# Performance work log

Hardware: AMD Instinct MI355X
Metric: run time of the kernel (lower is better)

## Reference

```python
import jax, jax.numpy as jnp
import numpy as np

B, V, F = 128, 256, 64      # batch, vertices, features-per-vertex
NS, NLR, K, NOUT = 4, 64, 40, 128
F_EFF = 2 * F               # cat_means doubles feature dim


def setup_inputs() -> dict:
    key = jax.random.key(0)
    k0, k1, k2 = jax.random.split(key, 3)
    x = jax.random.normal(k0, (B, V, F), dtype=jnp.float32)
    # f_slr: single Linear(F_EFF, NS+NLR) + ReLU (f_slr_depth=1)
    W_slr = jax.random.normal(k1, (F_EFF, NS + NLR), dtype=jnp.float32) / np.sqrt(F_EFF).astype(np.float32)
    b_slr = jnp.zeros((NS + NLR,), dtype=jnp.float32)
    # f_out: single Linear(F_EFF + 2*NLR, NOUT) + ReLU (f_out_depth=1, 2 agg methods)
    fin = F_EFF + 2 * NLR
    W_out = jax.random.normal(k2, (fin, NOUT), dtype=jnp.float32) / np.sqrt(fin).astype(np.float32)
    b_out = jnp.zeros((NOUT,), dtype=jnp.float32)
    return {"x": x, "W_slr": W_slr, "b_slr": b_slr, "W_out": W_out, "b_out": b_out}


def reference(x, W_slr, b_slr, W_out, b_out):
    # cat_means: append per-event feature means (broadcast over vertices)
    x = jnp.concatenate([x, jnp.broadcast_to(x.mean(axis=1, keepdims=True), x.shape)], axis=-1)  # (B,V,2F)
    slr = jax.nn.relu(x @ W_slr + b_slr)                    # (B,V,NS+NLR)
    s, lr = slr[..., :NS], slr[..., NS:]
    # pairwise squared distances in latent space (potential only needs d^2, so
    # we skip the sqrt: exp(-10*d^2) == exp(-10*d2), and kNN order is identical)
    diff = s[:, :, None, :] - s[:, None, :, :]              # (B,V,V,NS)
    d2 = jnp.sum(diff * diff, axis=-1)                      # (B,V,V)
    _, idx = jax.lax.top_k(-d2, K)                          # (B,V,K) k smallest (incl. self)
    d2k = jnp.take_along_axis(d2, idx, axis=2)              # (B,V,K)
    lr_nb = jax.vmap(lambda l, i: l[i])(lr, idx)            # (B,V,K,NLR)
    v = jnp.exp(-10.0 * d2k)                                # potential exp(-10 d^2)
    ft = lr_nb * v[..., None]                               # (B,V,K,NLR)
    fp = jnp.concatenate([x, ft.mean(axis=2), ft.max(axis=2)], axis=-1)  # (B,V,2F+2NLR)
    return jax.nn.relu(fp @ W_out + b_out)                  # (B,V,NOUT)
```

## Files before the change

kernel.cpp:

```cpp
#include <hip/hip_runtime.h>

constexpr int Bn = 128, Vn = 256, Fn = 64;
constexpr int NSLR = 68, NSn = 4, NLRn = 64;
constexpr int Kn = 40, NOUTn = 128;
constexpr int ROWS = Bn * Vn;
constexpr int KB2 = 192;

typedef __attribute__((ext_vector_type(8))) short short8;
typedef __attribute__((ext_vector_type(4))) float f32x4;

__device__ __forceinline__ int mbcnt64(unsigned long long m) {
  return __builtin_amdgcn_mbcnt_hi((unsigned)(m >> 32),
         __builtin_amdgcn_mbcnt_lo((unsigned)(m & 0xFFFFFFFFull), 0));
}
__device__ __forceinline__ unsigned short rneb(float v) {
  unsigned u = __float_as_uint(v);
  unsigned r = u + 0x7FFFu + ((u >> 16) & 1u);
  return (unsigned short)(r >> 16);
}
__device__ __forceinline__ float bf2f(unsigned short h) {
  return __uint_as_float(((unsigned)h) << 16);
}
#define GL_LDS(gp, lp) __builtin_amdgcn_global_load_lds( \
    (const __attribute__((address_space(1))) void*)(gp), \
    (__attribute__((address_space(3))) void*)(lp), 16, 0, 0)

__global__ __launch_bounds__(256) void kprep(
    const float* __restrict__ x,
    const float* __restrict__ W_slr, const float* __restrict__ b_slr,
    const float* __restrict__ W_out, const float* __restrict__ b_out,
    short* __restrict__ xhi, short* __restrict__ xlo,
    short* __restrict__ wt1h, short* __restrict__ wt1l, short* __restrict__ wt2,
    float* __restrict__ bias1, float* __restrict__ bias2) {
  const int blk = blockIdx.x, t = threadIdx.x;
  if (blk >= Bn) {
    const int col = blk - Bn;
    if (t < 64) {
      float val = (col < NSLR) ? W_slr[t * NSLR + col] : 0.f;
      unsigned short h = rneb(val);
      wt1h[col * 64 + t] = (short)h;
      wt1l[col * 64 + t] = (short)rneb(val - bf2f(h));
    } else {
      int k = t - 64;
      int row = (k < 64) ? k : 64 + k;
      wt2[col * KB2 + k] = (short)rneb(W_out[row * NOUTn + col]);
    }
    return;
  }
  const int b = blk;
  const int f4 = t & 15, vg = t >> 4;
  const float4* xb = (const float4*)(x + (size_t)b * 16384);
  float4 sum = make_float4(0.f, 0.f, 0.f, 0.f);
  for (int i = 0; i < 16; ++i) {
    int v = vg * 16 + i;
    float4 val = xb[v * 16 + f4];
    sum.x += val.x; sum.y += val.y; sum.z += val.z; sum.w += val.w;
    unsigned short h0 = rneb(val.x), h1 = rneb(val.y), h2 = rneb(val.z), h3 = rneb(val.w);
    short4 hi = {(short)h0, (short)h1, (short)h2, (short)h3};
    short4 lo = {(short)rneb(val.x - bf2f(h0)), (short)rneb(val.y - bf2f(h1)),
                 (short)rneb(val.z - bf2f(h2)), (short)rneb(val.w - bf2f(h3))};
    size_t o = (size_t)b * 4096 + v * 16 + f4;
    ((short4*)xhi)[o] = hi;
    ((short4*)xlo)[o] = lo;
  }
  __shared__ float4 ps[16][16];
  __shared__ float xms[64];
  ps[vg][f4] = sum;
  __syncthreads();
  if (t < 16) {
    float4 m = ps[0][t];
    for (int g = 1; g < 16; ++g) {
      float4 v = ps[g][t];
      m.x += v.x; m.y += v.y; m.z += v.z; m.w += v.w;
    }
    m.x *= (1.f / 256.f); m.y *= (1.f / 256.f); m.z *= (1.f / 256.f); m.w *= (1.f / 256.f);
    ((float4*)xms)[t] = m;
  }
  __syncthreads();
  if (t < 128) {
    float acc = b_out[t];
    for (int f = 0; f < 64; ++f) acc = fmaf(xms[f], W_out[(64 + f) * NOUTn + t], acc);
    bias2[b * 128 + t] = acc;
  } else {
    int c = t - 128;
    if (c < NSLR) {
      float acc = b_slr[c];
      for (int f = 0; f < 64; ++f) acc = fmaf(xms[f], W_slr[(64 + f) * NSLR + c], acc);
      bias1[b * 128 + c] = acc;
    }
  }
}

__global__ __launch_bounds__(256) void kgemm1(
    const short* __restrict__ xhi, const short* __restrict__ xlo,
    const short* __restrict__ wt1h, const short* __restrict__ wt1l,
    const float* __restrict__ bias1,
    float* __restrict__ s_ws, float* __restrict__ lr_ws) {
  __shared__ __align__(16) short Ah[4096], Al[4096], Bh[8192], Bl[1024];
  const int t = threadIdx.x, l = t & 63, w = t >> 6;
  const int wr = w >> 1, wc = w & 1;
  const int rowBase = blockIdx.x * 64;
  const int b = rowBase >> 8;
  const int lr8 = l >> 3, ul = (l & 7) ^ lr8;

#pragma unroll
  for (int rep = 0; rep < 2; ++rep) {
    const int seg = w + rep * 4;
    size_t o = (size_t)(rowBase + seg * 8 + lr8) * 64 + ul * 8;
    GL_LDS(xhi + o, &Ah[seg * 512]);
    GL_LDS(xlo + o, &Al[seg * 512]);
  }
#pragma unroll
  for (int rep = 0; rep < 4; ++rep) {
    const int seg = w + rep * 4;
    size_t o = (size_t)(seg * 8 + lr8) * 64 + ul * 8;
    GL_LDS(wt1h + o, &Bh[seg * 512]);
  }
  if (w < 2) {
    size_t o = (size_t)(w * 8 + lr8) * 64 + ul * 8;
    GL_LDS(wt1l + o, &Bl[w * 512]);
  }
  __syncthreads();

  f32x4 acc[2][4];
#pragma unroll
  for (int mf = 0; mf < 2; ++mf)
#pragma unroll
    for (int nf = 0; nf < 4; ++nf) acc[mf][nf] = (f32x4)(0.f);

#pragma unroll
  for (int ks = 0; ks < 2; ++ks) {
    short8 ah[2], bh[4];
#pragma unroll
    for (int mf = 0; mf < 2; ++mf) {
      int row = wr * 32 + mf * 16 + (l & 15);
      int pu = (ks * 4 + (l >> 4)) ^ (row & 7);
      ah[mf] = *(const short8*)&Ah[row * 64 + pu * 8];
    }
#pragma unroll
    for (int nf = 0; nf < 4; ++nf) {
      int col = wc * 64 + nf * 16 + (l & 15);
      int pu = (ks * 4 + (l >> 4)) ^ (col & 7);
      bh[nf] = *(const short8*)&Bh[col * 64 + pu * 8];
    }
#pragma unroll
    for (int mf = 0; mf < 2; ++mf)
#pragma unroll
      for (int nf = 0; nf < 4; ++nf)
        acc[mf][nf] = __builtin_amdgcn_mfma_f32_16x16x32_bf16(ah[mf], bh[nf], acc[mf][nf], 0, 0, 0);
    if (wc == 0) {
      int col0 = l & 15;
      int puc = (ks * 4 + (l >> 4)) ^ (col0 & 7);
      short8 bl0 = *(const short8*)&Bl[col0 * 64 + puc * 8];
#pragma unroll
      for (int mf = 0; mf < 2; ++mf) {
        int row = wr * 32 + mf * 16 + (l & 15);
        int pu = (ks * 4 + (l >> 4)) ^ (row & 7);
        short8 al = *(const short8*)&Al[row * 64 + pu * 8];
        acc[mf][0] = __builtin_amdgcn_mfma_f32_16x16x32_bf16(ah[mf], bl0, acc[mf][0], 0, 0, 0);
        acc[mf][0] = __builtin_amdgcn_mfma_f32_16x16x32_bf16(al, bh[0], acc[mf][0], 0, 0, 0);
      }
    }
  }
#pragma unroll
  for (int mf = 0; mf < 2; ++mf)
#pragma unroll
    for (int nf = 0; nf < 4; ++nf) {
      const int col = wc * 64 + nf * 16 + (l & 15);
      if (col < NSLR) {
        const float bia = bias1[b * 128 + col];
#pragma unroll
        for (int r = 0; r < 4; ++r) {
          int row = rowBase + wr * 32 + mf * 16 + (l >> 4) * 4 + r;
          float vv = acc[mf][nf][r] + bia;
          vv = vv > 0.f ? vv : 0.f;
          if (col < NSn) s_ws[b * 1024 + col * 256 + (row & 255)] = vv;
          else           lr_ws[(size_t)row * NLRn + (col - NSn)] = vv;
        }
      }
    }
}

__global__ __launch_bounds__(256) void kgemm2(
    const short* __restrict__ xhi, const short* __restrict__ fm,
    const short* __restrict__ fx, const short* __restrict__ wt2,
    const float* __restrict__ bias2, float* __restrict__ outp) {
  __shared__ __align__(16) short As[4096], Bs[8192];
  const int t = threadIdx.x, l = t & 63, w = t >> 6;
  const int wr = w >> 1, wc = w & 1;
  const int rowBase = blockIdx.x * 64;
  const int b = rowBase >> 8;
  const int lr8 = l >> 3, ul = (l & 7) ^ lr8;

  f32x4 acc[2][4];
#pragma unroll
  for (int mf = 0; mf < 2; ++mf)
#pragma unroll
    for (int nf = 0; nf < 4; ++nf) acc[mf][nf] = (f32x4)(0.f);

#pragma unroll
  for (int kc = 0; kc < 3; ++kc) {
    __syncthreads();
    const short* asrc = (kc == 0) ? xhi : (kc == 1) ? fm : fx;
#pragma unroll
    for (int rep = 0; rep < 2; ++rep) {
      const int seg = w + rep * 4;
      size_t o = (size_t)(rowBase + seg * 8 + lr8) * 64 + ul * 8;
      GL_LDS(asrc + o, &As[seg * 512]);
    }
#pragma unroll
    for (int rep = 0; rep < 4; ++rep) {
      const int seg = w + rep * 4;
      size_t o = (size_t)(seg * 8 + lr8) * KB2 + kc * 64 + ul * 8;
      GL_LDS(wt2 + o, &Bs[seg * 512]);
    }
    __syncthreads();
#pragma unroll
    for (int ks = 0; ks < 2; ++ks) {
      short8 a[2], bb[4];
#pragma unroll
      for (int mf = 0; mf < 2; ++mf) {
        int row = wr * 32 + mf * 16 + (l & 15);
        int pu = (ks * 4 + (l >> 4)) ^ (row & 7);
        a[mf] = *(const short8*)&As[row * 64 + pu * 8];
      }
#pragma unroll
      for (int nf = 0; nf < 4; ++nf) {
        int col = wc * 64 + nf * 16 + (l & 15);
        int pu = (ks * 4 + (l >> 4)) ^ (col & 7);
        bb[nf] = *(const short8*)&Bs[col * 64 + pu * 8];
      }
#pragma unroll
      for (int mf = 0; mf < 2; ++mf)
#pragma unroll
        for (int nf = 0; nf < 4; ++nf)
          acc[mf][nf] = __builtin_amdgcn_mfma_f32_16x16x32_bf16(a[mf], bb[nf], acc[mf][nf], 0, 0, 0);
    }
  }
#pragma unroll
  for (int mf = 0; mf < 2; ++mf)
#pragma unroll
    for (int nf = 0; nf < 4; ++nf) {
      const int col = wc * 64 + nf * 16 + (l & 15);
      const float bia = bias2[b * 128 + col];
#pragma unroll
      for (int r = 0; r < 4; ++r) {
        int row = rowBase + wr * 32 + mf * 16 + (l >> 4) * 4 + r;
        float vv = acc[mf][nf][r] + bia;
        outp[(size_t)row * NOUTn + col] = vv > 0.f ? vv : 0.f;
      }
    }
}

__device__ __forceinline__ int cntlt(const unsigned* kbr, unsigned c) {
  return __popcll(__ballot(kbr[0] < c)) + __popcll(__ballot(kbr[1] < c)) +
         __popcll(__ballot(kbr[2] < c)) + __popcll(__ballot(kbr[3] < c));
}

__global__ __launch_bounds__(256) void kselect(const float* __restrict__ s_ws,
                                               const float* __restrict__ lr_ws,
                                               short* __restrict__ fm,
                                               short* __restrict__ fx) {
  __shared__ float sT[4][256];
  __shared__ unsigned int lst[4][4][Kn];
  const int id = blockIdx.x;
  const int xcd = id & 7;
  const int rrx = id >> 3;
  const int b = xcd + 8 * (rrx & 15);
  const int seg = rrx >> 4;
  const int t = threadIdx.x, lane = t & 63, w = t >> 6;

  {
    const float* sb = s_ws + b * 1024;
    sT[0][t] = sb[t]; sT[1][t] = sb[256 + t];
    sT[2][t] = sb[512 + t]; sT[3][t] = sb[768 + t];
  }
  __syncthreads();

  float sj[4][4];
#pragma unroll
  for (int q = 0; q < 4; ++q)
#pragma unroll
    for (int c = 0; c < 4; ++c) sj[q][c] = sT[c][q * 64 + lane];

  const float C = -14.4269504088896340736f;
  unsigned kb[4][4];
  float vv[4][4];
#pragma unroll
  for (int r = 0; r < 4; ++r) {
    const int i = seg * 16 + w * 4 + r;
    const float si0 = sT[0][i], si1 = sT[1][i], si2 = sT[2][i], si3 = sT[3][i];
#pragma unroll
    for (int q = 0; q < 4; ++q) {
      float d0 = sj[q][0] - si0;
      float d1 = sj[q][1] - si1;
      float d2_ = sj[q][2] - si2;
      float d3 = sj[q][3] - si3;
      float dd = ((d0 * d0 + d1 * d1) + d2_ * d2_) + d3 * d3;
      kb[r][q] = __float_as_uint(dd);
      vv[r][q] = exp2f(C * dd);
    }
  }
  unsigned T[4] = {0u, 0u, 0u, 0u};
#pragma unroll 1
  for (int bit = 30; bit >= 0; --bit) {
    const unsigned m = 1u << bit;
    unsigned c0 = T[0] | m, c1 = T[1] | m, c2 = T[2] | m, c3 = T[3] | m;
    int n0 = cntlt(kb[0], c0);
    int n1 = cntlt(kb[1], c1);
    int n2 = cntlt(kb[2], c2);
    int n3 = cntlt(kb[3], c3);
    T[0] = (n0 < Kn) ? c0 : T[0];
    T[1] = (n1 < Kn) ? c1 : T[1];
    T[2] = (n2 < Kn) ? c2 : T[2];
    T[3] = (n3 < Kn) ? c3 : T[3];
  }
#pragma unroll
  for (int r = 0; r < 4; ++r) {
    const unsigned Tr = T[r];
    int nlt = cntlt(kb[r], Tr);
    int rem = Kn - nlt;
    int base = 0, ecum = 0;
#pragma unroll
    for (int q = 0; q < 4; ++q) {
      bool lt = kb[r][q] < Tr;
      bool eq = kb[r][q] == Tr;
      unsigned long long meq = __ballot(eq);
      int eqrank = ecum + mbcnt64(meq);
      bool sel = lt || (eq && (eqrank < rem));
      unsigned long long msel = __ballot(sel);
      int pos = base + mbcnt64(msel);
      if (sel)
        lst[w][r][pos] = (__float_as_uint(vv[r][q]) & 0xFFFFFF00u) | (unsigned)(q * 64 + lane);
      base += __popcll(msel);
      ecum += __popcll(meq);
    }
  }
  float accm[4] = {0.f, 0.f, 0.f, 0.f};
  float accx[4] = {0.f, 0.f, 0.f, 0.f};
  const float* lrb = lr_ws + (size_t)b * (256 * NLRn) + lane;
#pragma unroll 4
  for (int tt = 0; tt < Kn; ++tt) {
#pragma unroll
    for (int r = 0; r < 4; ++r) {
      unsigned p = lst[w][r][tt];
      int j = p & 0xFF;
      float v = __uint_as_float(p & 0xFFFFFF00u);
      float tv = v * lrb[j * NLRn];
      accm[r] += tv;
      accx[r] = fmaxf(accx[r], tv);
    }
  }
#pragma unroll
  for (int r = 0; r < 4; ++r) {
    const int i = seg * 16 + w * 4 + r;
    size_t ro = ((size_t)(b * 256 + i)) * 64 + lane;
    fm[ro] = (short)rneb(accm[r] * (1.f / 40.f));
    fx[ro] = (short)rneb(accx[r]);
  }
}

extern "C" void kernel_launch(void* const* d_in, const int* in_sizes, int n_in,
                              void* d_out, int out_size, void* d_ws, size_t ws_size,
                              hipStream_t stream) {
  const float* x = (const float*)d_in[0];
  const float* W_slr = (const float*)d_in[1];
  const float* b_slr = (const float*)d_in[2];
  const float* W_out = (const float*)d_in[3];
  const float* b_out = (const float*)d_in[4];
  float* out = (float*)d_out;

  char* p = (char*)d_ws;
  auto take = [&](size_t bytes) { char* c = p; p += (bytes + 255) & ~(size_t)255; return c; };
  short* xhi = (short*)take((size_t)ROWS * 64 * 2);
  short* xlo = (short*)take((size_t)ROWS * 64 * 2);
  short* wt1h = (short*)take(128 * 64 * 2);
  short* wt1l = (short*)take(128 * 64 * 2);
  short* wt2 = (short*)take(128 * KB2 * 2);
  float* bias1 = (float*)take(Bn * 128 * 4);
  float* bias2 = (float*)take(Bn * 128 * 4);
  float* s_ws = (float*)take(Bn * 1024 * 4);
  float* lr_ws = (float*)take((size_t)ROWS * 64 * 4);
  short* fm = (short*)take((size_t)ROWS * 64 * 2);
  short* fx = (short*)take((size_t)ROWS * 64 * 2);

  kprep<<<256, 256, 0, stream>>>(x, W_slr, b_slr, W_out, b_out,
                                 xhi, xlo, wt1h, wt1l, wt2, bias1, bias2);
  kgemm1<<<ROWS / 64, 256, 0, stream>>>(xhi, xlo, wt1h, wt1l, bias1, s_ws, lr_ws);
  kselect<<<Bn * 16, 256, 0, stream>>>(s_ws, lr_ws, fm, fx);
  kgemm2<<<ROWS / 64, 256, 0, stream>>>(xhi, fm, fx, wt2, bias2, out);
}
```

Baseline: 130.6 us.

## Store lr features as bf16, stage them in LDS for kNN gather, prefetch all gemm2 K-chunks

kgemm1 now writes the lr latent features as bf16 instead of fp32, which halves that intermediate's size. kselect copies the whole per-batch bf16 lr block (32 KB) into LDS with async global-to-LDS loads and gathers neighbours from LDS. Each lane processes two packed features for half-wave rows and writes packed bf16 pairs. kgemm2 loads all three K chunks into separate LDS buffers up front with a single barrier instead of two barriers per chunk. This trades extra LDS use, which may lower occupancy, and some lr precision for less global traffic and synchronisation.

```diff
diff --git a/kernel.cpp b/kernel.cpp
--- a/kernel.cpp
+++ b/kernel.cpp
@@ -95,7 +95,7 @@
     const short* __restrict__ xhi, const short* __restrict__ xlo,
     const short* __restrict__ wt1h, const short* __restrict__ wt1l,
     const float* __restrict__ bias1,
-    float* __restrict__ s_ws, float* __restrict__ lr_ws) {
+    float* __restrict__ s_ws, unsigned short* __restrict__ lr_bf) {
   __shared__ __align__(16) short Ah[4096], Al[4096], Bh[8192], Bl[1024];
   const int t = threadIdx.x, l = t & 63, w = t >> 6;
   const int wr = w >> 1, wc = w & 1;
@@ -175,7 +175,7 @@
           float vv = acc[mf][nf][r] + bia;
           vv = vv > 0.f ? vv : 0.f;
           if (col < NSn) s_ws[b * 1024 + col * 256 + (row & 255)] = vv;
-          else           lr_ws[(size_t)row * NLRn + (col - NSn)] = vv;
+          else           lr_bf[(size_t)row * NLRn + (col - NSn)] = rneb(vv);
         }
       }
     }
@@ -185,36 +185,39 @@
     const short* __restrict__ xhi, const short* __restrict__ fm,
     const short* __restrict__ fx, const short* __restrict__ wt2,
     const float* __restrict__ bias2, float* __restrict__ outp) {
-  __shared__ __align__(16) short As[4096], Bs[8192];
+  __shared__ __align__(16) short As[3][4096], Bs[3][8192];
   const int t = threadIdx.x, l = t & 63, w = t >> 6;
   const int wr = w >> 1, wc = w & 1;
   const int rowBase = blockIdx.x * 64;
   const int b = rowBase >> 8;
   const int lr8 = l >> 3, ul = (l & 7) ^ lr8;
 
-  f32x4 acc[2][4];
-#pragma unroll
-  for (int mf = 0; mf < 2; ++mf)
-#pragma unroll
-    for (int nf = 0; nf < 4; ++nf) acc[mf][nf] = (f32x4)(0.f);
-
 #pragma unroll
   for (int kc = 0; kc < 3; ++kc) {
-    __syncthreads();
     const short* asrc = (kc == 0) ? xhi : (kc == 1) ? fm : fx;
 #pragma unroll
     for (int rep = 0; rep < 2; ++rep) {
       const int seg = w + rep * 4;
       size_t o = (size_t)(rowBase + seg * 8 + lr8) * 64 + ul * 8;
-      GL_LDS(asrc + o, &As[seg * 512]);
+      GL_LDS(asrc + o, &As[kc][seg * 512]);
     }
 #pragma unroll
     for (int rep = 0; rep < 4; ++rep) {
       const int seg = w + rep * 4;
       size_t o = (size_t)(seg * 8 + lr8) * KB2 + kc * 64 + ul * 8;
-      GL_LDS(wt2 + o, &Bs[seg * 512]);
-    }
-    __syncthreads();
+      GL_LDS(wt2 + o, &Bs[kc][seg * 512]);
+    }
+  }
+  __syncthreads();
+
+  f32x4 acc[2][4];
+#pragma unroll
+  for (int mf = 0; mf < 2; ++mf)
+#pragma unroll
+    for (int nf = 0; nf < 4; ++nf) acc[mf][nf] = (f32x4)(0.f);
+
+#pragma unroll
+  for (int kc = 0; kc < 3; ++kc) {
 #pragma unroll
     for (int ks = 0; ks < 2; ++ks) {
       short8 a[2], bb[4];
@@ -222,13 +225,13 @@
       for (int mf = 0; mf < 2; ++mf) {
         int row = wr * 32 + mf * 16 + (l & 15);
         int pu = (ks * 4 + (l >> 4)) ^ (row & 7);
-        a[mf] = *(const short8*)&As[row * 64 + pu * 8];
+        a[mf] = *(const short8*)&As[kc][row * 64 + pu * 8];
       }
 #pragma unroll
       for (int nf = 0; nf < 4; ++nf) {
         int col = wc * 64 + nf * 16 + (l & 15);
         int pu = (ks * 4 + (l >> 4)) ^ (col & 7);
-        bb[nf] = *(const short8*)&Bs[col * 64 + pu * 8];
+        bb[nf] = *(const short8*)&Bs[kc][col * 64 + pu * 8];
       }
 #pragma unroll
       for (int mf = 0; mf < 2; ++mf)
@@ -258,10 +261,11 @@
 }
 
 __global__ __launch_bounds__(256) void kselect(const float* __restrict__ s_ws,
-                                               const float* __restrict__ lr_ws,
-                                               short* __restrict__ fm,
-                                               short* __restrict__ fx) {
+                                               const unsigned short* __restrict__ lr_bf,
+                                               unsigned* __restrict__ fm32,
+                                               unsigned* __restrict__ fx32) {
   __shared__ float sT[4][256];
+  __shared__ __align__(16) unsigned short lrs[16384];
   __shared__ unsigned int lst[4][4][Kn];
   const int id = blockIdx.x;
   const int xcd = id & 7;
@@ -271,6 +275,10 @@
   const int t = threadIdx.x, lane = t & 63, w = t >> 6;
 
   {
+    const unsigned short* lrg = lr_bf + (size_t)b * (256 * NLRn);
+#pragma unroll
+    for (int it = 0; it < 8; ++it)
+      GL_LDS(lrg + (it * 256 + t) * 8, &lrs[(it * 256 + t) * 8]);
     const float* sb = s_ws + b * 1024;
     sT[0][t] = sb[t]; sT[1][t] = sb[256 + t];
     sT[2][t] = sb[512 + t]; sT[3][t] = sb[768 + t];
@@ -336,27 +344,29 @@
       ecum += __popcll(meq);
     }
   }
-  float accm[4] = {0.f, 0.f, 0.f, 0.f};
-  float accx[4] = {0.f, 0.f, 0.f, 0.f};
-  const float* lrb = lr_ws + (size_t)b * (256 * NLRn) + lane;
+  const int h = lane >> 5;
+  const int f2 = lane & 31;
+#pragma unroll
+  for (int p = 0; p < 2; ++p) {
+    const unsigned* lstp = &lst[w][2 * p + h][0];
+    float am0 = 0.f, am1 = 0.f, ax0 = 0.f, ax1 = 0.f;
 #pragma unroll 4
-  for (int tt = 0; tt < Kn; ++tt) {
-#pragma unroll
-    for (int r = 0; r < 4; ++r) {
-      unsigned p = lst[w][r][tt];
-      int j = p & 0xFF;
-      float v = __uint_as_float(p & 0xFFFFFF00u);
-      float tv = v * lrb[j * NLRn];
-      accm[r] += tv;
-      accx[r] = fmaxf(accx[r], tv);
-    }
-  }
-#pragma unroll
-  for (int r = 0; r < 4; ++r) {
-    const int i = seg * 16 + w * 4 + r;
-    size_t ro = ((size_t)(b * 256 + i)) * 64 + lane;
-    fm[ro] = (short)rneb(accm[r] * (1.f / 40.f));
-    fx[ro] = (short)rneb(accx[r]);
+    for (int tt = 0; tt < Kn; ++tt) {
+      unsigned pk = lstp[tt];
+      float v = __uint_as_float(pk & 0xFFFFFF00u);
+      unsigned off = (pk & 0xFFu) << 6;
+      unsigned pr = *(const unsigned*)&lrs[off + f2 * 2];
+      float l0 = __uint_as_float(pr << 16);
+      float l1 = __uint_as_float(pr & 0xFFFF0000u);
+      float t0 = v * l0, t1 = v * l1;
+      am0 += t0; am1 += t1;
+      ax0 = fmaxf(ax0, t0); ax1 = fmaxf(ax1, t1);
+    }
+    const int i = seg * 16 + w * 4 + 2 * p + h;
+    size_t ro = ((size_t)(b * 256 + i)) * 32 + f2;
+    am0 *= (1.f / 40.f); am1 *= (1.f / 40.f);
+    fm32[ro] = (unsigned)rneb(am0) | ((unsigned)rneb(am1) << 16);
+    fx32[ro] = (unsigned)rneb(ax0) | ((unsigned)rneb(ax1) << 16);
   }
 }
 
@@ -380,13 +390,13 @@
   float* bias1 = (float*)take(Bn * 128 * 4);
   float* bias2 = (float*)take(Bn * 128 * 4);
   float* s_ws = (float*)take(Bn * 1024 * 4);
-  float* lr_ws = (float*)take((size_t)ROWS * 64 * 4);
+  unsigned short* lr_bf = (unsigned short*)take((size_t)ROWS * 64 * 2);
   short* fm = (short*)take((size_t)ROWS * 64 * 2);
   short* fx = (short*)take((size_t)ROWS * 64 * 2);
 
   kprep<<<256, 256, 0, stream>>>(x, W_slr, b_slr, W_out, b_out,
                                  xhi, xlo, wt1h, wt1l, wt2, bias1, bias2);
-  kgemm1<<<ROWS / 64, 256, 0, stream>>>(xhi, xlo, wt1h, wt1l, bias1, s_ws, lr_ws);
-  kselect<<<Bn * 16, 256, 0, stream>>>(s_ws, lr_ws, fm, fx);
+  kgemm1<<<ROWS / 64, 256, 0, stream>>>(xhi, xlo, wt1h, wt1l, bias1, s_ws, lr_bf);
+  kselect<<<Bn * 16, 256, 0, stream>>>(s_ws, lr_bf, (unsigned*)fm, (unsigned*)fx);
   kgemm2<<<ROWS / 64, 256, 0, stream>>>(xhi, fm, fx, wt2, bias2, out);
 }
```

Result: no change. 133.0 us (+1.8%).
